# Optimization experiments

Measured on AMD Instinct MI355X. Metric: run time of the kernel, lower is better.

The kernel has to match this reference:

```python
import jax, jax.numpy as jnp
import numpy as np

NUM_LEVELS = 4
RADIUS = 4


def _avg_pool2(x):
    # x: [B,S,C,H,W] -> 2x2 average pool, stride 2
    B, S, C, H, W = x.shape
    return x.reshape(B, S, C, H // 2, 2, W // 2, 2).mean(axis=(4, 6))


def _bilinear_sample(corr, x, y):
    # corr: [B,S,N,H,W]; x,y: [B,S,N,K,K] pixel coords; zeros padding, align_corners=True
    B, S, N, H, W = corr.shape
    corr_flat = corr.reshape(B, S, N, H * W)
    x0f = jnp.floor(x)
    y0f = jnp.floor(y)
    x0 = x0f.astype(jnp.int32)
    y0 = y0f.astype(jnp.int32)
    x1 = x0 + 1
    y1 = y0 + 1
    wx1 = x - x0f
    wx0 = 1.0 - wx1
    wy1 = y - y0f
    wy0 = 1.0 - wy1

    def gather(ix, iy):
        valid = ((ix >= 0) & (ix < W) & (iy >= 0) & (iy < H)).astype(corr.dtype)
        idx = jnp.clip(iy, 0, H - 1) * W + jnp.clip(ix, 0, W - 1)
        flat_idx = idx.reshape(B, S, N, -1)
        v = jnp.take_along_axis(corr_flat, flat_idx, axis=-1).reshape(ix.shape)
        return v * valid

    return (gather(x0, y0) * wx0 * wy0 + gather(x1, y0) * wx1 * wy0 +
            gather(x0, y1) * wx0 * wy1 + gather(x1, y1) * wx1 * wy1)


def _forward(features, targets, coordinates):
    B, S, C, H, W = features.shape
    N = targets.shape[2]
    inv_sqrt_c = 1.0 / jnp.sqrt(jnp.asarray(C, jnp.float32))

    # build feature pyramid
    pyramid = [features]
    f = features
    for _ in range(NUM_LEVELS - 1):
        f = _avg_pool2(f)
        pyramid.append(f)

    # correlate + windowed sample per level
    K = 2 * RADIUS + 1
    d = jnp.linspace(-RADIUS, RADIUS, K, dtype=jnp.float32)
    # faithful to torch: stack(meshgrid(dy, dx, indexing='ij'), -1)
    dyy, dxx = jnp.meshgrid(d, d, indexing='ij')
    delta = jnp.stack([dyy, dxx], axis=-1)  # [K,K,2]

    out_pyramid = []
    for i, feats in enumerate(pyramid):
        _, _, _, Hi, Wi = feats.shape
        # correlation volume [B,S,N,Hi,Wi]
        corr = jnp.einsum('bsnc,bschw->bsnhw', targets, feats) * inv_sqrt_c
        # window centers at this level
        centroid = coordinates[:, :, :, None, None, :] / (2.0 ** i)  # [B,S,N,1,1,2]
        pts = centroid + delta  # [B,S,N,K,K,2]; [...,0]=x, [...,1]=y (split order in torch code)
        sampled = _bilinear_sample(corr, pts[..., 0], pts[..., 1])  # [B,S,N,K,K]
        out_pyramid.append(sampled.reshape(B, S, N, K * K))

    return jnp.concatenate(out_pyramid, axis=-1)  # [B,S,N,NUM_LEVELS*K*K]


def setup_inputs() -> dict:
    key = jax.random.key(0)
    k1, k2, k3 = jax.random.split(key, 3)
    B, S, C, H, W = 1, 2, 128, 64, 96
    N = H * W
    features = jax.random.normal(k1, (B, S, C, H, W), dtype=jnp.float32)
    targets = jax.random.normal(k2, (B, S, N, C), dtype=jnp.float32)
    u = jax.random.uniform(k3, (B, S, N, 2), dtype=jnp.float32)
    scale = jnp.asarray([W - 1, H - 1], jnp.float32)  # x in [0,W-1], y in [0,H-1]
    coordinates = u * scale
    return {"features": features, "targets": targets, "coordinates": coordinates}


def reference(features, targets, coordinates):
    return _forward(features, targets, coordinates)
```

## Files before the change

### kernel.cpp

```cpp
#include <hip/hip_runtime.h>
#include <hip/hip_bf16.h>

#define SDIM 2
#define NPT  6144
#define CDIM 128
#define H0   64
#define W0   96

__constant__ int c_lvl_off[4] = {0, 786432, 983040, 1032192};

__device__ __forceinline__ float bf_lo(unsigned u) { return __uint_as_float(u << 16); }
__device__ __forceinline__ float bf_hi(unsigned u) { return __uint_as_float(u & 0xffff0000u); }

__device__ __forceinline__ unsigned pack_bf16(float a, float b) {
    unsigned ua = __float_as_uint(a);
    ua = (ua + 0x7fffu + ((ua >> 16) & 1u)) >> 16;
    unsigned ub = __float_as_uint(b);
    ub = (ub + 0x7fffu + ((ub >> 16) & 1u)) >> 16;
    return ua | (ub << 16);
}

__global__ __launch_bounds__(256) void transpose_kernel(const float* __restrict__ feat,
                                                        unsigned* __restrict__ out) {
    __shared__ float lds[64 * 129];
    const int bid = blockIdx.x;
    const int s = bid / 96;
    const int p0 = (bid % 96) * 64;
    const int tid = threadIdx.x;
    const int sub = tid >> 6;
    const int lane = tid & 63;
#pragma unroll
    for (int k = 0; k < 32; ++k) {
        int c = sub + k * 4;
        lds[lane * 129 + c] = feat[(s * CDIM + c) * (H0 * W0) + p0 + lane];
    }
    __syncthreads();
#pragma unroll
    for (int k = 0; k < 16; ++k) {
        int pl = sub + k * 4;
        float lo = lds[pl * 129 + lane * 2];
        float hi = lds[pl * 129 + lane * 2 + 1];
        out[(size_t)(s * (H0 * W0) + p0 + pl) * 64 + lane] = pack_bf16(lo, hi);
    }
}

__global__ __launch_bounds__(256) void pool_kernel(const unsigned* __restrict__ in,
                                                   unsigned* __restrict__ out,
                                                   int H2, int W2) {
    int idx = blockIdx.x * 256 + threadIdx.x;
    int total = SDIM * H2 * W2 * 64;
    if (idx >= total) return;
    int cp = idx & 63;
    int pix = idx >> 6;
    int x2 = pix % W2;
    int t = pix / W2;
    int y2 = t % H2;
    int s = t / H2;
    int W1 = W2 * 2;
    int base = ((s * (H2 * 2) + y2 * 2) * W1 + x2 * 2) * 64 + cp;
    int sy = W1 * 64;
    unsigned u00 = in[base], u01 = in[base + 64];
    unsigned u10 = in[base + sy], u11 = in[base + sy + 64];
    float lo = (bf_lo(u00) + bf_lo(u01) + bf_lo(u10) + bf_lo(u11)) * 0.25f;
    float hi = (bf_hi(u00) + bf_hi(u01) + bf_hi(u10) + bf_hi(u11)) * 0.25f;
    out[idx] = pack_bf16(lo, hi);
}

__global__ __launch_bounds__(256) void corr_kernel(const float* __restrict__ targets,
                                                   const float* __restrict__ coords,
                                                   const unsigned* __restrict__ pyr,
                                                   float* __restrict__ out) {
    __shared__ __align__(16) float tgt[CDIM];
    __shared__ float Ds[4][112];

    const int sn = blockIdx.x;
    const int tid = threadIdx.x;

    if (tid < CDIM) tgt[tid] = targets[(size_t)sn * CDIM + tid];
    const float cx = coords[sn * 2 + 0];
    const float cy = coords[sn * 2 + 1];
    __syncthreads();

    const int lvl = tid >> 6;
    const int lane = tid & 63;
    const int g = lane >> 2;
    const int k = lane & 3;

    const int Wi = W0 >> lvl;
    const int Hi = H0 >> lvl;
    const int s = sn / NPT;
    const unsigned* base = pyr + c_lvl_off[lvl] + s * Hi * Wi * 64;

    const float scale = 1.0f / (float)(1 << lvl);
    const float cxl = cx * scale, cyl = cy * scale;
    const float x0f = floorf(cxl), y0f = floorf(cyl);
    const float wx1 = cxl - x0f, wx0 = 1.0f - wx1;
    const float wy1 = cyl - y0f, wy0 = 1.0f - wy1;
    const int ix0 = (int)x0f - 4;
    const int iy0 = (int)y0f - 4;

    float treg[32];
#pragma unroll
    for (int q = 0; q < 8; ++q) {
        float4 v = *(const float4*)&tgt[k * 32 + q * 4];
        treg[q * 4 + 0] = v.x; treg[q * 4 + 1] = v.y;
        treg[q * 4 + 2] = v.z; treg[q * 4 + 3] = v.w;
    }

    for (int it = 0; it < 7; ++it) {
        int p = it * 16 + g;
        int row = (p * 205) >> 11;
        int col = p - row * 10;
        int y = iy0 + row;
        int x = ix0 + col;
        bool valid = ((unsigned)x < (unsigned)Wi) && ((unsigned)y < (unsigned)Hi);
        int xc = min(max(x, 0), Wi - 1);
        int yc = min(max(y, 0), Hi - 1);
        const uint4* ptr = (const uint4*)(base + (yc * Wi + xc) * 64 + k * 16);
        float acc = 0.0f;
#pragma unroll
        for (int q = 0; q < 4; ++q) {
            uint4 v = ptr[q];
            acc = fmaf(bf_lo(v.x), treg[q * 8 + 0], acc);
            acc = fmaf(bf_hi(v.x), treg[q * 8 + 1], acc);
            acc = fmaf(bf_lo(v.y), treg[q * 8 + 2], acc);
            acc = fmaf(bf_hi(v.y), treg[q * 8 + 3], acc);
            acc = fmaf(bf_lo(v.z), treg[q * 8 + 4], acc);
            acc = fmaf(bf_hi(v.z), treg[q * 8 + 5], acc);
            acc = fmaf(bf_lo(v.w), treg[q * 8 + 6], acc);
            acc = fmaf(bf_hi(v.w), treg[q * 8 + 7], acc);
        }
        acc += __shfl_xor(acc, 1);
        acc += __shfl_xor(acc, 2);
        if (k == 0 && p < 100) Ds[lvl][p] = valid ? acc : 0.0f;
    }

    __syncthreads();

    const float isc = 0.08838834764831843f;
    const size_t obase = (size_t)sn * 324 + lvl * 81;
#pragma unroll
    for (int r = 0; r < 2; ++r) {
        int o = r * 64 + lane;
        if (o < 81) {
            int j = (o * 57) >> 9;
            int i = o - j * 9;
            float d00 = Ds[lvl][i * 10 + j];
            float d01 = Ds[lvl][i * 10 + j + 1];
            float d10 = Ds[lvl][(i + 1) * 10 + j];
            float d11 = Ds[lvl][(i + 1) * 10 + j + 1];
            float v = wy0 * (wx0 * d00 + wx1 * d01) + wy1 * (wx0 * d10 + wx1 * d11);
            out[obase + o] = v * isc;
        }
    }
}

extern "C" void kernel_launch(void* const* d_in, const int* in_sizes, int n_in,
                              void* d_out, int out_size, void* d_ws, size_t ws_size,
                              hipStream_t stream) {
    const float* features = (const float*)d_in[0];
    const float* targets  = (const float*)d_in[1];
    const float* coords   = (const float*)d_in[2];
    float* out = (float*)d_out;

    unsigned* pyr = (unsigned*)d_ws;

    transpose_kernel<<<SDIM * (H0 * W0 / 64), 256, 0, stream>>>(features, pyr);

    pool_kernel<<<(SDIM * 32 * 48 * 64 + 255) / 256, 256, 0, stream>>>(
        pyr + 0,       pyr + 786432, 32, 48);
    pool_kernel<<<(SDIM * 16 * 24 * 64 + 255) / 256, 256, 0, stream>>>(
        pyr + 786432,  pyr + 983040, 16, 24);
    pool_kernel<<<(SDIM * 8 * 12 * 64 + 255) / 256, 256, 0, stream>>>(
        pyr + 983040,  pyr + 1032192, 8, 12);

    corr_kernel<<<SDIM * NPT, 256, 0, stream>>>(targets, coords, pyr, out);
}
```

Baseline: 152.7 us.

## Switch pyramid to fp16 with packed dot2 and fuse pool levels into one kernel

The feature pyramid is now stored as packed fp16 instead of bf16. The correlation inner loop uses v_dot2 packed fp16 dot products with two accumulators in place of unpacking and doing scalar FMAs. The three chained pooling launches become one kernel that averages each coarse level straight from level 0, which removes two launches and their serial dependency at the cost of more reads per output. Iterations with out-of-range points (p>=100) are skipped. Targets are rounded to fp16 with round-toward-zero, and fp16 has a narrower range than bf16, which may add precision risk.

```diff
diff --git a/kernel.cpp b/kernel.cpp
--- a/kernel.cpp
+++ b/kernel.cpp
@@ -7,17 +7,17 @@
 #define H0   64
 #define W0   96
 
+typedef __fp16 half2_t __attribute__((ext_vector_type(2)));
+
 __constant__ int c_lvl_off[4] = {0, 786432, 983040, 1032192};
 
-__device__ __forceinline__ float bf_lo(unsigned u) { return __uint_as_float(u << 16); }
-__device__ __forceinline__ float bf_hi(unsigned u) { return __uint_as_float(u & 0xffff0000u); }
+__device__ __forceinline__ unsigned pack_f16(float a, float b) {
+    half2_t h = __builtin_amdgcn_cvt_pkrtz(a, b);
+    return __builtin_bit_cast(unsigned, h);
+}
 
-__device__ __forceinline__ unsigned pack_bf16(float a, float b) {
-    unsigned ua = __float_as_uint(a);
-    ua = (ua + 0x7fffu + ((ua >> 16) & 1u)) >> 16;
-    unsigned ub = __float_as_uint(b);
-    ub = (ub + 0x7fffu + ((ub >> 16) & 1u)) >> 16;
-    return ua | (ub << 16);
+__device__ __forceinline__ half2_t as_h2(unsigned u) {
+    return __builtin_bit_cast(half2_t, u);
 }
 
 __global__ __launch_bounds__(256) void transpose_kernel(const float* __restrict__ feat,
@@ -40,30 +40,43 @@
         int pl = sub + k * 4;
         float lo = lds[pl * 129 + lane * 2];
         float hi = lds[pl * 129 + lane * 2 + 1];
-        out[(size_t)(s * (H0 * W0) + p0 + pl) * 64 + lane] = pack_bf16(lo, hi);
+        out[(size_t)(s * (H0 * W0) + p0 + pl) * 64 + lane] = pack_f16(lo, hi);
     }
 }
 
-__global__ __launch_bounds__(256) void pool_kernel(const unsigned* __restrict__ in,
-                                                   unsigned* __restrict__ out,
-                                                   int H2, int W2) {
+__global__ __launch_bounds__(256) void pool_all_kernel(const unsigned* __restrict__ pyr0,
+                                                       unsigned* __restrict__ pyr) {
     int idx = blockIdx.x * 256 + threadIdx.x;
-    int total = SDIM * H2 * W2 * 64;
-    if (idx >= total) return;
-    int cp = idx & 63;
-    int pix = idx >> 6;
-    int x2 = pix % W2;
-    int t = pix / W2;
-    int y2 = t % H2;
-    int s = t / H2;
-    int W1 = W2 * 2;
-    int base = ((s * (H2 * 2) + y2 * 2) * W1 + x2 * 2) * 64 + cp;
-    int sy = W1 * 64;
-    unsigned u00 = in[base], u01 = in[base + 64];
-    unsigned u10 = in[base + sy], u11 = in[base + sy + 64];
-    float lo = (bf_lo(u00) + bf_lo(u01) + bf_lo(u10) + bf_lo(u11)) * 0.25f;
-    float hi = (bf_hi(u00) + bf_hi(u01) + bf_hi(u10) + bf_hi(u11)) * 0.25f;
-    out[idx] = pack_bf16(lo, hi);
+    int lvl, rem;
+    if (idx < 196608)      { lvl = 1; rem = idx; }
+    else if (idx < 245760) { lvl = 2; rem = idx - 196608; }
+    else if (idx < 258048) { lvl = 3; rem = idx - 245760; }
+    else return;
+
+    const int m = 1 << lvl;
+    const int Wi = W0 >> lvl;
+    const int Hi = H0 >> lvl;
+    const int cp = rem & 63;
+    const int pix = rem >> 6;
+    const int x = pix % Wi;
+    const int t = pix / Wi;
+    const int y = t % Hi;
+    const int s = t / Hi;
+
+    const int row_stride = W0 * 64;
+    const unsigned* base = pyr0 + ((s * H0 + y * m) * W0 + x * m) * 64 + cp;
+
+    float lo = 0.0f, hi = 0.0f;
+    for (int dy = 0; dy < m; ++dy) {
+        const unsigned* rp = base + dy * row_stride;
+        for (int dx = 0; dx < m; ++dx) {
+            half2_t v = as_h2(rp[dx * 64]);
+            lo += (float)v.x;
+            hi += (float)v.y;
+        }
+    }
+    const float inv = 1.0f / (float)(m * m);
+    pyr[c_lvl_off[lvl] + rem] = pack_f16(lo * inv, hi * inv);
 }
 
 __global__ __launch_bounds__(256) void corr_kernel(const float* __restrict__ targets,
@@ -99,40 +112,36 @@
     const int ix0 = (int)x0f - 4;
     const int iy0 = (int)y0f - 4;
 
-    float treg[32];
+    half2_t treg[16];
 #pragma unroll
-    for (int q = 0; q < 8; ++q) {
-        float4 v = *(const float4*)&tgt[k * 32 + q * 4];
-        treg[q * 4 + 0] = v.x; treg[q * 4 + 1] = v.y;
-        treg[q * 4 + 2] = v.z; treg[q * 4 + 3] = v.w;
-    }
+    for (int q = 0; q < 16; ++q)
+        treg[q] = __builtin_amdgcn_cvt_pkrtz(tgt[k * 32 + 2 * q], tgt[k * 32 + 2 * q + 1]);
 
     for (int it = 0; it < 7; ++it) {
         int p = it * 16 + g;
-        int row = (p * 205) >> 11;
-        int col = p - row * 10;
-        int y = iy0 + row;
-        int x = ix0 + col;
-        bool valid = ((unsigned)x < (unsigned)Wi) && ((unsigned)y < (unsigned)Hi);
-        int xc = min(max(x, 0), Wi - 1);
-        int yc = min(max(y, 0), Hi - 1);
-        const uint4* ptr = (const uint4*)(base + (yc * Wi + xc) * 64 + k * 16);
-        float acc = 0.0f;
+        if (p < 100) {
+            int row = (p * 205) >> 11;
+            int col = p - row * 10;
+            int y = iy0 + row;
+            int x = ix0 + col;
+            bool valid = ((unsigned)x < (unsigned)Wi) && ((unsigned)y < (unsigned)Hi);
+            int xc = min(max(x, 0), Wi - 1);
+            int yc = min(max(y, 0), Hi - 1);
+            const uint4* ptr = (const uint4*)(base + (yc * Wi + xc) * 64 + k * 16);
+            float acc0 = 0.0f, acc1 = 0.0f;
 #pragma unroll
-        for (int q = 0; q < 4; ++q) {
-            uint4 v = ptr[q];
-            acc = fmaf(bf_lo(v.x), treg[q * 8 + 0], acc);
-            acc = fmaf(bf_hi(v.x), treg[q * 8 + 1], acc);
-            acc = fmaf(bf_lo(v.y), treg[q * 8 + 2], acc);
-            acc = fmaf(bf_hi(v.y), treg[q * 8 + 3], acc);
-            acc = fmaf(bf_lo(v.z), treg[q * 8 + 4], acc);
-            acc = fmaf(bf_hi(v.z), treg[q * 8 + 5], acc);
-            acc = fmaf(bf_lo(v.w), treg[q * 8 + 6], acc);
-            acc = fmaf(bf_hi(v.w), treg[q * 8 + 7], acc);
+            for (int q = 0; q < 4; ++q) {
+                uint4 v = ptr[q];
+                acc0 = __builtin_amdgcn_fdot2(as_h2(v.x), treg[q * 4 + 0], acc0, false);
+                acc1 = __builtin_amdgcn_fdot2(as_h2(v.y), treg[q * 4 + 1], acc1, false);
+                acc0 = __builtin_amdgcn_fdot2(as_h2(v.z), treg[q * 4 + 2], acc0, false);
+                acc1 = __builtin_amdgcn_fdot2(as_h2(v.w), treg[q * 4 + 3], acc1, false);
+            }
+            float acc = acc0 + acc1;
+            acc += __shfl_xor(acc, 1);
+            acc += __shfl_xor(acc, 2);
+            if (k == 0) Ds[lvl][p] = valid ? acc : 0.0f;
         }
-        acc += __shfl_xor(acc, 1);
-        acc += __shfl_xor(acc, 2);
-        if (k == 0 && p < 100) Ds[lvl][p] = valid ? acc : 0.0f;
     }
 
     __syncthreads();
@@ -167,12 +176,7 @@
 
     transpose_kernel<<<SDIM * (H0 * W0 / 64), 256, 0, stream>>>(features, pyr);
 
-    pool_kernel<<<(SDIM * 32 * 48 * 64 + 255) / 256, 256, 0, stream>>>(
-        pyr + 0,       pyr + 786432, 32, 48);
-    pool_kernel<<<(SDIM * 16 * 24 * 64 + 255) / 256, 256, 0, stream>>>(
-        pyr + 786432,  pyr + 983040, 16, 24);
-    pool_kernel<<<(SDIM * 8 * 12 * 64 + 255) / 256, 256, 0, stream>>>(
-        pyr + 983040,  pyr + 1032192, 8, 12);
+    pool_all_kernel<<<(258048 + 255) / 256, 256, 0, stream>>>(pyr, pyr);
 
     corr_kernel<<<SDIM * NPT, 256, 0, stream>>>(targets, coords, pyr, out);
 }
```

After: 163.2 us. 1.07x slower.
